# Kernel optimization log

Measured on AMD Instinct MI355X. Metric: run time of the kernel, lower is better.

The kernel has to match this reference:

```python
import jax, jax.numpy as jnp
import numpy as np

B, N, H, NH = 2, 2048, 256, 8
D = H // NH           # head dim = 32
SPATIAL = NH * 7      # 3 points + 1 distance + 3 direction per head
LN_EPS = 1e-5


def layer_norm(x, g, b):
    m = jnp.mean(x, axis=-1, keepdims=True)
    v = jnp.mean(jnp.square(x - m), axis=-1, keepdims=True)
    return (x - m) * jax.lax.rsqrt(v + LN_EPS) * g + b


def setup_inputs() -> dict:
    key = jax.random.key(0)
    ks = jax.random.split(key, 12)
    s = 0.02
    return {
        "x": jax.random.normal(ks[0], (B, N, H), jnp.float32),
        "pos_CA": jax.random.normal(ks[1], (B, N, 3), jnp.float32),
        "pos_CB": jax.random.normal(ks[2], (B, N, 3), jnp.float32),
        "frame": jax.random.normal(ks[3], (B, N, 3, 3), jnp.float32),
        "mask": jnp.ones((B, N), dtype=bool),
        # linear weights stored [in, out] so y = x @ W + b
        "Wq": jax.random.normal(ks[4], (H, H), jnp.float32) * s,
        "bq": jnp.zeros((H,), jnp.float32),
        "Wk": jax.random.normal(ks[5], (H, H), jnp.float32) * s,
        "bk": jnp.zeros((H,), jnp.float32),
        "Wv": jax.random.normal(ks[6], (H, H), jnp.float32) * s,
        "bv": jnp.zeros((H,), jnp.float32),
        "W_out": jax.random.normal(ks[7], (H + SPATIAL, H), jnp.float32) * s,
        "b_out": jnp.zeros((H,), jnp.float32),
        "ln1_g": jnp.ones((H,), jnp.float32),
        "ln1_b": jnp.zeros((H,), jnp.float32),
        "ln2_g": jnp.ones((H,), jnp.float32),
        "ln2_b": jnp.zeros((H,), jnp.float32),
    }


def reference(x, pos_CA, pos_CB, frame, mask, Wq, bq, Wk, bk, Wv, bv,
              W_out, b_out, ln1_g, ln1_b, ln2_g, ln2_b):
    b, n, hdim = x.shape
    q = (x @ Wq + bq).reshape(b, n, NH, D)
    k = (x @ Wk + bk).reshape(b, n, NH, D)
    v = (x @ Wv + bv).reshape(b, n, NH, D)

    # logits [b, l, k, h] (note: no 1/sqrt(d) scaling in the original)
    logits = jnp.einsum('blhd,bkhd->blkh', q, k)
    m2 = (mask[:, :, None] & mask[:, None, :])[..., None]  # [b,l,k,1]
    logits = jnp.where(m2, logits, -jnp.inf)
    alpha = jax.nn.softmax(logits, axis=2)  # softmax over k

    feat_node = jnp.einsum('blkh,bkhd->blhd', alpha, v).reshape(b, n, hdim)

    # rel_pos[b,l,k] = CB[l] - CA[k]
    rel_pos = pos_CB[:, :, None, :] - pos_CA[:, None, :, :]  # [b,l,k,3]
    atom_pos_bias = jnp.einsum('blkh,blkd->blhd', alpha, rel_pos)  # [b,l,h,3]

    feat_distance = jnp.linalg.norm(atom_pos_bias, axis=-1, keepdims=True)  # [b,l,h,1]
    feat_points = jnp.einsum('blij,blhj->blhi', frame, atom_pos_bias)       # [b,l,h,3]
    feat_direction = feat_points / (
        jnp.linalg.norm(feat_points, axis=-1, keepdims=True) + 1e-10)

    feat_spatial = jnp.concatenate([
        feat_points.reshape(b, n, NH * 3),
        feat_distance.reshape(b, n, NH),
        feat_direction.reshape(b, n, NH * 3),
    ], axis=-1)

    feat_all = jnp.concatenate([feat_node, feat_spatial], axis=-1)
    y = jax.nn.relu(feat_all @ W_out + b_out)
    y = layer_norm(y, ln1_g, ln1_b)
    y = jnp.where(mask[..., None], y, 0.0)
    # hidden dims match -> residual path
    return layer_norm(x + y, ln2_g, ln2_b)
```

## Files before the change

kernel.cpp:

```cpp
#include <hip/hip_runtime.h>
#include <hip/hip_bf16.h>
#include <math.h>

#define B_ 2
#define N_ 2048
#define H_ 256
#define NH_ 8
#define D_ 32
#define FEAT_ 312
#define FEATP_ 320

typedef __attribute__((ext_vector_type(8))) short bf16x8;
typedef __attribute__((ext_vector_type(4))) short s16x4;
typedef __attribute__((ext_vector_type(4))) float f32x4;

__device__ __forceinline__ short f2bf(float f) {
    unsigned int u = __float_as_uint(f);
    unsigned int r = (u + 0x7fffu + ((u >> 16) & 1u)) >> 16;
    return (short)(unsigned short)r;
}

__global__ __launch_bounds__(256) void prep_kernel(
    const float* __restrict__ x, const float* __restrict__ Wq,
    const float* __restrict__ Wk, const float* __restrict__ Wv,
    const float* __restrict__ Wout, const float* __restrict__ pos_CA,
    short* __restrict__ xb, short* __restrict__ Wt, short* __restrict__ Wot,
    short* __restrict__ caT, short* __restrict__ featb)
{
    const int t = blockIdx.x * 256 + threadIdx.x;
    for (int i = t; i < (B_ * N_ * H_) / 4; i += 65536) {
        float4 v = *(const float4*)(x + (size_t)i * 4);
        s16x4 o;
        o[0] = f2bf(v.x); o[1] = f2bf(v.y); o[2] = f2bf(v.z); o[3] = f2bf(v.w);
        *(s16x4*)(xb + (size_t)i * 4) = o;
    }
    for (int i = t; i < 768 * 256; i += 65536) {
        int n = i >> 8, kk = i & 255;
        int region = n >> 8, nn = n & 255;
        const float* W = region == 0 ? Wq : (region == 1 ? Wk : Wv);
        Wt[i] = f2bf(W[kk * 256 + nn]);
    }
    for (int i = t; i < 256 * FEATP_; i += 65536) {
        int n = i / FEATP_, kk = i % FEATP_;
        Wot[i] = f2bf(kk < FEAT_ ? Wout[kk * 256 + n] : 0.f);
    }
    if (t < 6 * N_) {
        int d6 = t >> 11, n = t & (N_ - 1);
        int bb = d6 / 3, dd = d6 % 3;
        caT[t] = f2bf(pos_CA[((size_t)bb * N_ + n) * 3 + dd]);
    }
    if (t < B_ * N_ * 8) {
        int l = t >> 3, c = FEAT_ + (t & 7);
        featb[(size_t)l * FEATP_ + c] = 0;
    }
}

__global__ __launch_bounds__(256) void qkv_gemm(
    const short* __restrict__ xb, const short* __restrict__ Wt,
    const float* __restrict__ bq, const float* __restrict__ bk,
    const float* __restrict__ bv,
    short* __restrict__ qb, short* __restrict__ kb, short* __restrict__ vT)
{
    const int wave = threadIdx.x >> 6, lane = threadIdx.x & 63;
    const int quad = lane >> 4, col = lane & 15;
    const int n0 = blockIdx.x * 128 + (wave & 1) * 64;
    const int m0 = blockIdx.y * 64 + (wave >> 1) * 32;

    f32x4 acc[2][4];
#pragma unroll
    for (int i = 0; i < 2; ++i)
#pragma unroll
        for (int j = 0; j < 4; ++j) acc[i][j] = (f32x4){0.f, 0.f, 0.f, 0.f};

#pragma unroll
    for (int k0 = 0; k0 < 256; k0 += 32) {
        bf16x8 af[2], bfr[4];
#pragma unroll
        for (int i = 0; i < 2; ++i)
            af[i] = *(const bf16x8*)(xb + (size_t)(m0 + i * 16 + col) * 256 + k0 + quad * 8);
#pragma unroll
        for (int j = 0; j < 4; ++j)
            bfr[j] = *(const bf16x8*)(Wt + (size_t)(n0 + j * 16 + col) * 256 + k0 + quad * 8);
#pragma unroll
        for (int i = 0; i < 2; ++i)
#pragma unroll
            for (int j = 0; j < 4; ++j)
                acc[i][j] = __builtin_amdgcn_mfma_f32_16x16x32_bf16(af[i], bfr[j], acc[i][j], 0, 0, 0);
    }

    const int region = blockIdx.x >> 1;
    const float* bias = region == 0 ? bq : (region == 1 ? bk : bv);
    float bo[4];
#pragma unroll
    for (int j = 0; j < 4; ++j) bo[j] = bias[(n0 + j * 16 + col) & 255];

    if (region < 2) {
        short* dst = region == 0 ? qb : kb;
#pragma unroll
        for (int i = 0; i < 2; ++i)
#pragma unroll
            for (int j = 0; j < 4; ++j)
#pragma unroll
                for (int r = 0; r < 4; ++r)
                    dst[(size_t)(m0 + i * 16 + quad * 4 + r) * 256 +
                        ((n0 + j * 16 + col) & 255)] = f2bf(acc[i][j][r] + bo[j]);
    } else {
#pragma unroll
        for (int i = 0; i < 2; ++i) {
            const int gl0 = m0 + i * 16 + quad * 4;
            const int bb = gl0 >> 11, l0 = gl0 & (N_ - 1);
#pragma unroll
            for (int j = 0; j < 4; ++j) {
                const int vcol = (n0 + j * 16 + col) & 255;
                const int hh = vcol >> 5, dd = vcol & 31;
                s16x4 pk;
#pragma unroll
                for (int r = 0; r < 4; ++r) pk[r] = f2bf(acc[i][j][r] + bo[j]);
                *(s16x4*)(vT + (size_t)((bb * 8 + hh) * 32 + dd) * N_ + l0) = pk;
            }
        }
    }
}

__global__ __launch_bounds__(512) void attn_kernel(
    const short* __restrict__ qg, const short* __restrict__ kgb,
    const short* __restrict__ vTg, const short* __restrict__ caT,
    const float* __restrict__ pos_CB, const float* __restrict__ frame,
    short* __restrict__ featb)
{
    const int bx = blockIdx.x;
    const int lt = bx & 31, h = (bx >> 5) & 7, b = bx >> 8;
    const int tid = threadIdx.x;
    const int wave = tid >> 6, lane = tid & 63;
    const int kg = wave >> 2, wl = wave & 3;
    const int quad = lane >> 4, col = lane & 15;

    __shared__ short Ks[2][2][64 * 40];
    __shared__ short VT[2][2][48 * 72];
    __shared__ short Pw[8][16 * 72];
    __shared__ float Obuf[4][16][40];

    for (int i = tid; i < 4 * 13 * 72; i += 512) {
        int plane = i / (13 * 72), r = i % (13 * 72);
        VT[plane >> 1][plane & 1][35 * 72 + r] = 0;
    }

    const int l_base = lt * 64 + wl * 16;
    const bf16x8 qfrag =
        *(const bf16x8*)(qg + ((size_t)(b * N_ + l_base + col)) * H_ + h * D_ + quad * 8);

    f32x4 accO[3];
#pragma unroll
    for (int dt = 0; dt < 3; ++dt) accO[dt] = (f32x4){0.f, 0.f, 0.f, 0.f};
    float srun = 0.f;

    const short* kbase = kgb + (size_t)(b * N_) * H_ + h * D_;
    const short* vTb = vTg + (size_t)((b * 8 + h) * 32) * N_;
    const short* caTb = caT + (size_t)(b * 3) * N_;

    const int local = tid & 255;
    const int krow = local >> 2, seg = local & 3;
    const int vd = local >> 3, vseg = local & 7;
    const int cad = local >> 6, cak = local & 63;
    const int kofs = kg * 1024;

    float4 kreg = *(const float4*)(kbase + (size_t)(kofs + krow) * H_ + seg * 8);
    float4 vreg = *(const float4*)(vTb + (size_t)vd * N_ + kofs + vseg * 8);
    short careg = (local < 192) ? caTb[(size_t)cad * N_ + kofs + cak] : (short)0;

    int buf = 0;
    for (int it = 0; it < 16; ++it) {
        *(float4*)&Ks[kg][buf][krow * 40 + seg * 8] = kreg;
        *(float4*)&VT[kg][buf][vd * 72 + vseg * 8] = vreg;
        if (local < 192) VT[kg][buf][(32 + cad) * 72 + cak] = careg;
        __syncthreads();

        if (it < 15) {
            const int k0 = kofs + (it + 1) * 64;
            kreg = *(const float4*)(kbase + (size_t)(k0 + krow) * H_ + seg * 8);
            vreg = *(const float4*)(vTb + (size_t)vd * N_ + k0 + vseg * 8);
            if (local < 192) careg = caTb[(size_t)cad * N_ + k0 + cak];
        }

        float p16[16];
        float sr0 = 0.f, sr1 = 0.f;
#pragma unroll
        for (int t = 0; t < 4; ++t) {
            const bf16x8 kfrag = *(const bf16x8*)&Ks[kg][buf][(t * 16 + col) * 40 + quad * 8];
            f32x4 z4 = (f32x4){0.f, 0.f, 0.f, 0.f};
            f32x4 s = __builtin_amdgcn_mfma_f32_16x16x32_bf16(kfrag, qfrag, z4, 0, 0, 0);
            float e0 = __expf(s[0]), e1 = __expf(s[1]);
            float e2 = __expf(s[2]), e3 = __expf(s[3]);
            p16[t * 4 + 0] = e0; p16[t * 4 + 1] = e1;
            p16[t * 4 + 2] = e2; p16[t * 4 + 3] = e3;
            sr0 += e0 + e1; sr1 += e2 + e3;
        }
        srun += sr0 + sr1;
#pragma unroll
        for (int t = 0; t < 4; ++t) {
            __hip_bfloat162 pa = __float22bfloat162_rn(make_float2(p16[t * 4 + 0], p16[t * 4 + 1]));
            __hip_bfloat162 pb = __float22bfloat162_rn(make_float2(p16[t * 4 + 2], p16[t * 4 + 3]));
            uint2 pk;
            pk.x = *(unsigned int*)&pa;
            pk.y = *(unsigned int*)&pb;
            *(uint2*)&Pw[wave][col * 72 + t * 16 + quad * 4] = pk;
        }
#pragma unroll
        for (int half = 0; half < 2; ++half) {
            const bf16x8 pfrag =
                *(const bf16x8*)&Pw[wave][col * 72 + half * 32 + quad * 8];
#pragma unroll
            for (int dt = 0; dt < 3; ++dt) {
                const bf16x8 vfrag =
                    *(const bf16x8*)&VT[kg][buf][(dt * 16 + col) * 72 + half * 32 + quad * 8];
                accO[dt] = __builtin_amdgcn_mfma_f32_16x16x32_bf16(pfrag, vfrag, accO[dt], 0, 0, 0);
            }
        }
        buf ^= 1;
    }

    srun += __shfl_xor(srun, 16);
    srun += __shfl_xor(srun, 32);

    if (kg == 1) {
#pragma unroll
        for (int dt = 0; dt < 2; ++dt)
#pragma unroll
            for (int r = 0; r < 4; ++r)
                Obuf[wl][quad * 4 + r][dt * 16 + col] = accO[dt][r];
        if (col < 3)
#pragma unroll
            for (int r = 0; r < 4; ++r)
                Obuf[wl][quad * 4 + r][32 + col] = accO[2][r];
        if (quad == 0) Obuf[wl][col][35] = srun;
    }
    __syncthreads();
    if (kg == 0) {
        if (quad == 0) Obuf[wl][col][35] += srun;
        float inv[4];
#pragma unroll
        for (int r = 0; r < 4; ++r) inv[r] = 1.f / Obuf[wl][quad * 4 + r][35];

#pragma unroll
        for (int dt = 0; dt < 2; ++dt)
#pragma unroll
            for (int r = 0; r < 4; ++r) {
                float o = (accO[dt][r] + Obuf[wl][quad * 4 + r][dt * 16 + col]) * inv[r];
                featb[(size_t)(b * N_ + l_base + quad * 4 + r) * FEATP_ +
                      h * D_ + dt * 16 + col] = f2bf(o);
            }
        if (col < 3)
#pragma unroll
            for (int r = 0; r < 4; ++r)
                Obuf[wl][quad * 4 + r][36 + col] =
                    (accO[2][r] + Obuf[wl][quad * 4 + r][32 + col]) * inv[r];

        if (lane < 16) {
            const int l = l_base + lane;
            const float ox = Obuf[wl][lane][36];
            const float oy = Obuf[wl][lane][37];
            const float oz = Obuf[wl][lane][38];
            const float* pcb = pos_CB + (size_t)(b * N_ + l) * 3;
            const float ax = pcb[0] - ox, ay = pcb[1] - oy, az = pcb[2] - oz;
            const float* fr = frame + (size_t)(b * N_ + l) * 9;
            const float p0 = fr[0] * ax + fr[1] * ay + fr[2] * az;
            const float p1 = fr[3] * ax + fr[4] * ay + fr[5] * az;
            const float p2 = fr[6] * ax + fr[7] * ay + fr[8] * az;
            const float dist = sqrtf(ax * ax + ay * ay + az * az);
            const float pn = sqrtf(p0 * p0 + p1 * p1 + p2 * p2);
            const float rinv = 1.f / (pn + 1e-10f);
            short* fb = featb + (size_t)(b * N_ + l) * FEATP_;
            fb[256 + h * 3 + 0] = f2bf(p0);
            fb[256 + h * 3 + 1] = f2bf(p1);
            fb[256 + h * 3 + 2] = f2bf(p2);
            fb[280 + h] = f2bf(dist);
            fb[288 + h * 3 + 0] = f2bf(p0 * rinv);
            fb[288 + h * 3 + 1] = f2bf(p1 * rinv);
            fb[288 + h * 3 + 2] = f2bf(p2 * rinv);
        }
    }
}

__global__ __launch_bounds__(256) void out_ln(
    const short* __restrict__ featb, const short* __restrict__ Wot,
    const float* __restrict__ bout, const float* __restrict__ x,
    const float* __restrict__ g1, const float* __restrict__ b1,
    const float* __restrict__ g2, const float* __restrict__ b2,
    float* __restrict__ out)
{
    const int wave = threadIdx.x >> 6, lane = threadIdx.x & 63;
    const int quad = lane >> 4, col = lane & 15;
    const int m0 = blockIdx.x * 16;
    const int n0 = wave * 64;

    f32x4 acc[4];
#pragma unroll
    for (int j = 0; j < 4; ++j) acc[j] = (f32x4){0.f, 0.f, 0.f, 0.f};

#pragma unroll
    for (int k0 = 0; k0 < FEATP_; k0 += 32) {
        const bf16x8 af = *(const bf16x8*)(featb + (size_t)(m0 + col) * FEATP_ + k0 + quad * 8);
#pragma unroll
        for (int j = 0; j < 4; ++j) {
            const bf16x8 bfr =
                *(const bf16x8*)(Wot + (size_t)(n0 + j * 16 + col) * FEATP_ + k0 + quad * 8);
            acc[j] = __builtin_amdgcn_mfma_f32_16x16x32_bf16(af, bfr, acc[j], 0, 0, 0);
        }
    }

    __shared__ float red[4][16][2];
    float yv[4][4], s[4], q2[4];
#pragma unroll
    for (int r = 0; r < 4; ++r) { s[r] = 0.f; q2[r] = 0.f; }
#pragma unroll
    for (int j = 0; j < 4; ++j) {
        const float bo = bout[n0 + j * 16 + col];
#pragma unroll
        for (int r = 0; r < 4; ++r) {
            float t = fmaxf(acc[j][r] + bo, 0.f);
            yv[j][r] = t; s[r] += t; q2[r] += t * t;
        }
    }
#pragma unroll
    for (int off = 1; off <= 8; off <<= 1)
#pragma unroll
        for (int r = 0; r < 4; ++r) {
            s[r] += __shfl_xor(s[r], off);
            q2[r] += __shfl_xor(q2[r], off);
        }
    if (col == 0)
#pragma unroll
        for (int r = 0; r < 4; ++r) {
            red[wave][quad * 4 + r][0] = s[r];
            red[wave][quad * 4 + r][1] = q2[r];
        }
    __syncthreads();

    float zv[4][4], s2[4], qq[4];
#pragma unroll
    for (int r = 0; r < 4; ++r) { s2[r] = 0.f; qq[r] = 0.f; }
    float mean1[4], rs1[4];
#pragma unroll
    for (int r = 0; r < 4; ++r) {
        const int row = quad * 4 + r;
        float S = red[0][row][0] + red[1][row][0] + red[2][row][0] + red[3][row][0];
        float Q = red[0][row][1] + red[1][row][1] + red[2][row][1] + red[3][row][1];
        mean1[r] = S * (1.f / 256.f);
        float var = Q * (1.f / 256.f) - mean1[r] * mean1[r];
        rs1[r] = rsqrtf(var + 1e-5f);
    }
#pragma unroll
    for (int j = 0; j < 4; ++j) {
        const int colg = n0 + j * 16 + col;
        const float g1v = g1[colg], b1v = b1[colg];
#pragma unroll
        for (int r = 0; r < 4; ++r) {
            float yn = (yv[j][r] - mean1[r]) * rs1[r] * g1v + b1v;
            float z = x[(size_t)(m0 + quad * 4 + r) * H_ + colg] + yn;
            zv[j][r] = z; s2[r] += z; qq[r] += z * z;
        }
    }
#pragma unroll
    for (int off = 1; off <= 8; off <<= 1)
#pragma unroll
        for (int r = 0; r < 4; ++r) {
            s2[r] += __shfl_xor(s2[r], off);
            qq[r] += __shfl_xor(qq[r], off);
        }
    __syncthreads();
    if (col == 0)
#pragma unroll
        for (int r = 0; r < 4; ++r) {
            red[wave][quad * 4 + r][0] = s2[r];
            red[wave][quad * 4 + r][1] = qq[r];
        }
    __syncthreads();
#pragma unroll
    for (int r = 0; r < 4; ++r) {
        const int row = quad * 4 + r;
        float S = red[0][row][0] + red[1][row][0] + red[2][row][0] + red[3][row][0];
        float Q = red[0][row][1] + red[1][row][1] + red[2][row][1] + red[3][row][1];
        float mean2 = S * (1.f / 256.f);
        float var2 = Q * (1.f / 256.f) - mean2 * mean2;
        float rs2 = rsqrtf(var2 + 1e-5f);
#pragma unroll
        for (int j = 0; j < 4; ++j) {
            const int colg = n0 + j * 16 + col;
            out[(size_t)(m0 + row) * H_ + colg] =
                (zv[j][r] - mean2) * rs2 * g2[colg] + b2[colg];
        }
    }
}

extern "C" void kernel_launch(void* const* d_in, const int* in_sizes, int n_in,
                              void* d_out, int out_size, void* d_ws, size_t ws_size,
                              hipStream_t stream) {
    const float* x      = (const float*)d_in[0];
    const float* pos_CA = (const float*)d_in[1];
    const float* pos_CB = (const float*)d_in[2];
    const float* frame  = (const float*)d_in[3];
    const float* Wq   = (const float*)d_in[5];
    const float* bq   = (const float*)d_in[6];
    const float* Wk   = (const float*)d_in[7];
    const float* bk   = (const float*)d_in[8];
    const float* Wv   = (const float*)d_in[9];
    const float* bv   = (const float*)d_in[10];
    const float* Wout = (const float*)d_in[11];
    const float* bout = (const float*)d_in[12];
    const float* g1   = (const float*)d_in[13];
    const float* b1   = (const float*)d_in[14];
    const float* g2   = (const float*)d_in[15];
    const float* b2   = (const float*)d_in[16];

    char* ws = (char*)d_ws;
    short* xb    = (short*)(ws);
    short* qb    = (short*)(ws + (2u << 20));
    short* kb    = (short*)(ws + (4u << 20));
    short* vT    = (short*)(ws + (6u << 20));
    short* Wt    = (short*)(ws + (8u << 20));
    short* Wot   = (short*)(ws + (8u << 20) + 393216);
    short* caT   = (short*)(ws + (8u << 20) + 557056);
    short* featb = (short*)(ws + (9u << 20));

    prep_kernel<<<256, 256, 0, stream>>>(x, Wq, Wk, Wv, Wout, pos_CA,
                                         xb, Wt, Wot, caT, featb);
    qkv_gemm<<<dim3(6, 64), 256, 0, stream>>>(xb, Wt, bq, bk, bv, qb, kb, vT);
    attn_kernel<<<512, 512, 0, stream>>>(qb, kb, vT, caT, pos_CB, frame, featb);
    out_ln<<<256, 256, 0, stream>>>(featb, Wot, bout, x, g1, b1, g2, b2,
                                    (float*)d_out);
}
```

Measured before the change: 142.1 us.

## Fuse x bf16 conversion into QKV GEMM and keep P in registers for PV MFMA

The separate bf16 conversion pass over x in the prep kernel is removed; the QKV GEMM now loads fp32 x directly and packs it to bf16 in registers. In the attention kernel, the softmax probabilities are no longer staged through per-wave shared memory. The PV product is reorganised as V^T·P using the 16x16x16 MFMA, so the S accumulator layout feeds the B operand directly, and the epilogue is rewritten for the transposed output layout. This drops an LDS round trip and a barrier-free shuffle per tile, at the cost of more, smaller MFMAs and double fp32 load traffic in the GEMM.

Result: no change. 143.9 us (+1.3%).

```diff
diff --git a/kernel.cpp b/kernel.cpp
--- a/kernel.cpp
+++ b/kernel.cpp
@@ -20,20 +20,23 @@
     return (short)(unsigned short)r;
 }
 
+__device__ __forceinline__ bf16x8 pack8(float4 a, float4 b) {
+    union { bf16x8 v; __hip_bfloat162 h[4]; } u;
+    u.h[0] = __float22bfloat162_rn(make_float2(a.x, a.y));
+    u.h[1] = __float22bfloat162_rn(make_float2(a.z, a.w));
+    u.h[2] = __float22bfloat162_rn(make_float2(b.x, b.y));
+    u.h[3] = __float22bfloat162_rn(make_float2(b.z, b.w));
+    return u.v;
+}
+
 __global__ __launch_bounds__(256) void prep_kernel(
-    const float* __restrict__ x, const float* __restrict__ Wq,
-    const float* __restrict__ Wk, const float* __restrict__ Wv,
-    const float* __restrict__ Wout, const float* __restrict__ pos_CA,
-    short* __restrict__ xb, short* __restrict__ Wt, short* __restrict__ Wot,
+    const float* __restrict__ Wq, const float* __restrict__ Wk,
+    const float* __restrict__ Wv, const float* __restrict__ Wout,
+    const float* __restrict__ pos_CA,
+    short* __restrict__ Wt, short* __restrict__ Wot,
     short* __restrict__ caT, short* __restrict__ featb)
 {
     const int t = blockIdx.x * 256 + threadIdx.x;
-    for (int i = t; i < (B_ * N_ * H_) / 4; i += 65536) {
-        float4 v = *(const float4*)(x + (size_t)i * 4);
-        s16x4 o;
-        o[0] = f2bf(v.x); o[1] = f2bf(v.y); o[2] = f2bf(v.z); o[3] = f2bf(v.w);
-        *(s16x4*)(xb + (size_t)i * 4) = o;
-    }
     for (int i = t; i < 768 * 256; i += 65536) {
         int n = i >> 8, kk = i & 255;
         int region = n >> 8, nn = n & 255;
@@ -56,7 +59,7 @@
 }
 
 __global__ __launch_bounds__(256) void qkv_gemm(
-    const short* __restrict__ xb, const short* __restrict__ Wt,
+    const float* __restrict__ x, const short* __restrict__ Wt,
     const float* __restrict__ bq, const float* __restrict__ bk,
     const float* __restrict__ bv,
     short* __restrict__ qb, short* __restrict__ kb, short* __restrict__ vT)
@@ -76,8 +79,10 @@
     for (int k0 = 0; k0 < 256; k0 += 32) {
         bf16x8 af[2], bfr[4];
 #pragma unroll
-        for (int i = 0; i < 2; ++i)
-            af[i] = *(const bf16x8*)(xb + (size_t)(m0 + i * 16 + col) * 256 + k0 + quad * 8);
+        for (int i = 0; i < 2; ++i) {
+            const float* xp = x + (size_t)(m0 + i * 16 + col) * 256 + k0 + quad * 8;
+            af[i] = pack8(*(const float4*)xp, *(const float4*)(xp + 4));
+        }
 #pragma unroll
         for (int j = 0; j < 4; ++j)
             bfr[j] = *(const bf16x8*)(Wt + (size_t)(n0 + j * 16 + col) * 256 + k0 + quad * 8);
@@ -137,8 +142,7 @@
 
     __shared__ short Ks[2][2][64 * 40];
     __shared__ short VT[2][2][48 * 72];
-    __shared__ short Pw[8][16 * 72];
-    __shared__ float Obuf[4][16][40];
+    __shared__ float Obuf[4][16][50];
 
     for (int i = tid; i < 4 * 13 * 72; i += 512) {
         int plane = i / (13 * 72), r = i % (13 * 72);
@@ -182,8 +186,7 @@
             if (local < 192) careg = caTb[(size_t)cad * N_ + k0 + cak];
         }
 
-        float p16[16];
-        float sr0 = 0.f, sr1 = 0.f;
+        s16x4 pbf[4];
 #pragma unroll
         for (int t = 0; t < 4; ++t) {
             const bf16x8 kfrag = *(const bf16x8*)&Ks[kg][buf][(t * 16 + col) * 40 + quad * 8];
@@ -191,29 +194,19 @@
             f32x4 s = __builtin_amdgcn_mfma_f32_16x16x32_bf16(kfrag, qfrag, z4, 0, 0, 0);
             float e0 = __expf(s[0]), e1 = __expf(s[1]);
             float e2 = __expf(s[2]), e3 = __expf(s[3]);
-            p16[t * 4 + 0] = e0; p16[t * 4 + 1] = e1;
-            p16[t * 4 + 2] = e2; p16[t * 4 + 3] = e3;
-            sr0 += e0 + e1; sr1 += e2 + e3;
-        }
-        srun += sr0 + sr1;
-#pragma unroll
-        for (int t = 0; t < 4; ++t) {
-            __hip_bfloat162 pa = __float22bfloat162_rn(make_float2(p16[t * 4 + 0], p16[t * 4 + 1]));
-            __hip_bfloat162 pb = __float22bfloat162_rn(make_float2(p16[t * 4 + 2], p16[t * 4 + 3]));
-            uint2 pk;
-            pk.x = *(unsigned int*)&pa;
-            pk.y = *(unsigned int*)&pb;
-            *(uint2*)&Pw[wave][col * 72 + t * 16 + quad * 4] = pk;
-        }
-#pragma unroll
-        for (int half = 0; half < 2; ++half) {
-            const bf16x8 pfrag =
-                *(const bf16x8*)&Pw[wave][col * 72 + half * 32 + quad * 8];
-#pragma unroll
-            for (int dt = 0; dt < 3; ++dt) {
-                const bf16x8 vfrag =
-                    *(const bf16x8*)&VT[kg][buf][(dt * 16 + col) * 72 + half * 32 + quad * 8];
-                accO[dt] = __builtin_amdgcn_mfma_f32_16x16x32_bf16(pfrag, vfrag, accO[dt], 0, 0, 0);
+            srun += (e0 + e1) + (e2 + e3);
+            union { s16x4 v; __hip_bfloat162 h[2]; } u;
+            u.h[0] = __float22bfloat162_rn(make_float2(e0, e1));
+            u.h[1] = __float22bfloat162_rn(make_float2(e2, e3));
+            pbf[t] = u.v;
+        }
+#pragma unroll
+        for (int dt = 0; dt < 3; ++dt) {
+            const short* vrow = &VT[kg][buf][(dt * 16 + col) * 72 + quad * 4];
+#pragma unroll
+            for (int t = 0; t < 4; ++t) {
+                const s16x4 afrag = *(const s16x4*)(vrow + t * 16);
+                accO[dt] = __builtin_amdgcn_mfma_f32_16x16x16bf16_1k(afrag, pbf[t], accO[dt], 0, 0, 0);
             }
         }
         buf ^= 1;
@@ -224,42 +217,28 @@
 
     if (kg == 1) {
 #pragma unroll
-        for (int dt = 0; dt < 2; ++dt)
+        for (int dt = 0; dt < 3; ++dt)
 #pragma unroll
             for (int r = 0; r < 4; ++r)
-                Obuf[wl][quad * 4 + r][dt * 16 + col] = accO[dt][r];
-        if (col < 3)
-#pragma unroll
-            for (int r = 0; r < 4; ++r)
-                Obuf[wl][quad * 4 + r][32 + col] = accO[2][r];
-        if (quad == 0) Obuf[wl][col][35] = srun;
+                Obuf[wl][col][dt * 16 + quad * 4 + r] = accO[dt][r];
+        if (lane < 16) Obuf[wl][lane][48] = srun;
     }
     __syncthreads();
     if (kg == 0) {
-        if (quad == 0) Obuf[wl][col][35] += srun;
-        float inv[4];
-#pragma unroll
-        for (int r = 0; r < 4; ++r) inv[r] = 1.f / Obuf[wl][quad * 4 + r][35];
-
-#pragma unroll
-        for (int dt = 0; dt < 2; ++dt)
-#pragma unroll
-            for (int r = 0; r < 4; ++r) {
-                float o = (accO[dt][r] + Obuf[wl][quad * 4 + r][dt * 16 + col]) * inv[r];
-                featb[(size_t)(b * N_ + l_base + quad * 4 + r) * FEATP_ +
-                      h * D_ + dt * 16 + col] = f2bf(o);
-            }
-        if (col < 3)
+        const float inv = 1.f / (srun + Obuf[wl][col][48]);
+        const int l = l_base + col;
+#pragma unroll
+        for (int dt = 0; dt < 2; ++dt) {
+            s16x4 pk;
 #pragma unroll
             for (int r = 0; r < 4; ++r)
-                Obuf[wl][quad * 4 + r][36 + col] =
-                    (accO[2][r] + Obuf[wl][quad * 4 + r][32 + col]) * inv[r];
-
-        if (lane < 16) {
-            const int l = l_base + lane;
-            const float ox = Obuf[wl][lane][36];
-            const float oy = Obuf[wl][lane][37];
-            const float oz = Obuf[wl][lane][38];
+                pk[r] = f2bf((accO[dt][r] + Obuf[wl][col][dt * 16 + quad * 4 + r]) * inv);
+            *(s16x4*)&featb[(size_t)(b * N_ + l) * FEATP_ + h * D_ + dt * 16 + quad * 4] = pk;
+        }
+        if (quad == 0) {
+            const float ox = (accO[2][0] + Obuf[wl][col][32]) * inv;
+            const float oy = (accO[2][1] + Obuf[wl][col][33]) * inv;
+            const float oz = (accO[2][2] + Obuf[wl][col][34]) * inv;
             const float* pcb = pos_CB + (size_t)(b * N_ + l) * 3;
             const float ax = pcb[0] - ox, ay = pcb[1] - oy, az = pcb[2] - oz;
             const float* fr = frame + (size_t)(b * N_ + l) * 9;
@@ -413,18 +392,17 @@
     const float* b2   = (const float*)d_in[16];
 
     char* ws = (char*)d_ws;
-    short* xb    = (short*)(ws);
-    short* qb    = (short*)(ws + (2u << 20));
-    short* kb    = (short*)(ws + (4u << 20));
-    short* vT    = (short*)(ws + (6u << 20));
-    short* Wt    = (short*)(ws + (8u << 20));
-    short* Wot   = (short*)(ws + (8u << 20) + 393216);
-    short* caT   = (short*)(ws + (8u << 20) + 557056);
-    short* featb = (short*)(ws + (9u << 20));
-
-    prep_kernel<<<256, 256, 0, stream>>>(x, Wq, Wk, Wv, Wout, pos_CA,
-                                         xb, Wt, Wot, caT, featb);
-    qkv_gemm<<<dim3(6, 64), 256, 0, stream>>>(xb, Wt, bq, bk, bv, qb, kb, vT);
+    short* qb    = (short*)(ws);
+    short* kb    = (short*)(ws + (2u << 20));
+    short* vT    = (short*)(ws + (4u << 20));
+    short* Wt    = (short*)(ws + (6u << 20));
+    short* Wot   = (short*)(ws + (6u << 20) + 393216);
+    short* caT   = (short*)(ws + (6u << 20) + 557056);
+    short* featb = (short*)(ws + (7u << 20));
+
+    prep_kernel<<<256, 256, 0, stream>>>(Wq, Wk, Wv, Wout, pos_CA,
+                                         Wt, Wot, caT, featb);
+    qkv_gemm<<<dim3(6, 64), 256, 0, stream>>>(x, Wt, bq, bk, bv, qb, kb, vT);
     attn_kernel<<<512, 512, 0, stream>>>(qb, kb, vT, caT, pos_CB, frame, featb);
     out_ln<<<256, 256, 0, stream>>>(featb, Wot, bout, x, g1, b1, g2, b2,
                                     (float*)d_out);
```
